# Performance work log

Measured on AMD Instinct MI355X. Metric: run time of the kernel, lower is better.

The kernel has to match this reference:

```python
import jax, jax.numpy as jnp
import numpy as np

K = 20        # kNN neighborhood size (args.k)
EPS = 1e-5    # BatchNorm eps
SLOPE = 0.2   # LeakyReLU negative slope
B, N = 8, 2048


def lrelu(x):
    return jnp.where(x >= 0, x, SLOPE * x)


def bn_cn(x):  # BatchNorm1d over [B, C, N] (training-mode batch stats, gamma=1, beta=0)
    m = jnp.mean(x, axis=(0, 2), keepdims=True)
    v = jnp.var(x, axis=(0, 2), keepdims=True)
    return (x - m) * jax.lax.rsqrt(v + EPS)


def bn_f(x):  # BatchNorm1d over [B, F]
    m = jnp.mean(x, axis=0, keepdims=True)
    v = jnp.var(x, axis=0, keepdims=True)
    return (x - m) * jax.lax.rsqrt(v + EPS)


def conv_bn(x, w):  # 1x1 Conv1d (no bias) + BN + LeakyReLU; x [B,C,N], w [O,C]
    return lrelu(bn_cn(jnp.einsum('oc,bcn->bon', w, x)))


def knn_idx(x, k):  # x [B,C,N] -> [B,N,k] nearest neighbors, self excluded
    sq = jnp.sum(x * x, axis=1)                                   # [B,N]
    pd = 2.0 * jnp.einsum('bcn,bcm->bnm', x, x) - sq[:, :, None] - sq[:, None, :]
    return jax.lax.top_k(pd, k + 1)[1][:, :, 1:]                  # drop self (max = 0)


def self_att(x, wq, wk, wv, wc):  # SelfAttention block (n_heads=1, scale_dot)
    idx = knn_idx(x, K)                                           # [B,N,K]
    feats = jnp.swapaxes(x, 1, 2)                                 # [B,N,C]
    nb = jax.vmap(lambda f, i: f[i])(feats, idx)                  # [B,N,K,C] gather
    E = wq.shape[0]
    q = feats @ wq.T                                              # [B,N,E]
    kk = nb @ wk.T                                                # [B,N,K,E]
    v = (nb - feats[:, :, None, :]) @ wv.T                        # [B,N,K,V]
    scores = jax.nn.softmax(jnp.einsum('bne,bnke->bnk', q, kk) / np.float32(np.sqrt(E)), axis=-1)
    out = jnp.einsum('bnk,bnkv->bnv', scores, v)                  # [B,N,V]
    res = conv_bn(jnp.swapaxes(out, 1, 2), wc)                    # [B,O,N]
    return jnp.concatenate([res, x], axis=1)


def setup_inputs() -> dict:
    key = jax.random.key(0)
    ks = jax.random.split(key, 32)
    w = lambda k, o, i: jax.random.normal(k, (o, i), jnp.float32) / np.float32(np.sqrt(i))
    d = {'x': jax.random.normal(ks[0], (B, 3, N), jnp.float32)}
    dims = {1: 3, 2: 64, 3: 64, 4: 128}
    j = 1
    for s, c in dims.items():
        for nm in ('wq', 'wk', 'wv', 'wc'):
            d[f'sa{s}_{nm}'] = w(ks[j], c, c); j += 1
    d['conv1_w'] = w(ks[17], 64, 6)
    d['conv2_w'] = w(ks[18], 64, 128)
    d['conv3_w'] = w(ks[19], 128, 128)
    d['conv4_w'] = w(ks[20], 256, 256)
    d['conv5_w'] = w(ks[21], 1024, 512)
    d['lin1_w'] = w(ks[22], 512, 2048); d['lin1_b'] = jnp.zeros((512,), jnp.float32)
    d['lin2_w'] = w(ks[23], 256, 512);  d['lin2_b'] = jnp.zeros((256,), jnp.float32)
    d['lin3_w'] = w(ks[24], 40, 256);   d['lin3_b'] = jnp.zeros((40,), jnp.float32)
    return d


def reference(x, sa1_wq, sa1_wk, sa1_wv, sa1_wc, sa2_wq, sa2_wk, sa2_wv, sa2_wc,
              sa3_wq, sa3_wk, sa3_wv, sa3_wc, sa4_wq, sa4_wk, sa4_wv, sa4_wc,
              conv1_w, conv2_w, conv3_w, conv4_w, conv5_w,
              lin1_w, lin1_b, lin2_w, lin2_b, lin3_w, lin3_b):
    h = self_att(x, sa1_wq, sa1_wk, sa1_wv, sa1_wc)        # [B,6,N]
    x1 = conv_bn(h, conv1_w)                               # [B,64,N]
    h = self_att(x1, sa2_wq, sa2_wk, sa2_wv, sa2_wc)       # [B,128,N]
    x2 = conv_bn(h, conv2_w)                               # [B,64,N]
    h = self_att(x2, sa3_wq, sa3_wk, sa3_wv, sa3_wc)       # [B,128,N]
    x3 = conv_bn(h, conv3_w)                               # [B,128,N]
    h = self_att(x3, sa4_wq, sa4_wk, sa4_wv, sa4_wc)       # [B,256,N]
    x4 = conv_bn(h, conv4_w)                               # [B,256,N]
    xc = jnp.concatenate([x1, x2, x3, x4], axis=1)         # [B,512,N]
    x5 = conv_bn(xc, conv5_w)                              # [B,1024,N]
    p = jnp.concatenate([jnp.max(x5, axis=2), jnp.mean(x5, axis=2)], axis=1)  # [B,2048]
    h = lrelu(bn_f(p @ lin1_w.T + lin1_b))                 # dropout = identity (eval)
    h = lrelu(bn_f(h @ lin2_w.T + lin2_b))
    return h @ lin3_w.T + lin3_b                           # [B,40]
```

## Files before the change

kernel.cpp:

```cpp
#include <hip/hip_runtime.h>
#include <math.h>

#define BB 8
#define NN 2048
#define KNB 20

typedef __attribute__((ext_vector_type(8))) short bf16x8;
typedef __attribute__((ext_vector_type(8))) _Float16 f16x8;
typedef __attribute__((ext_vector_type(4))) float f32x4;

__device__ inline unsigned short f2bf(float f) {
  union { float f; unsigned u; } v; v.f = f;
  unsigned r = v.u + 0x7FFF + ((v.u >> 16) & 1);
  return (unsigned short)(r >> 16);
}

__device__ inline float lrelu(float v) { return v >= 0.f ? v : 0.2f * v; }

template <bool F16SPLIT, bool BF16>
__global__ __launch_bounds__(256) void xprep_kernel(
    const float* __restrict__ in, int inBS, int C,
    float* __restrict__ xT, _Float16* __restrict__ hi, _Float16* __restrict__ lo,
    unsigned short* __restrict__ bf, float* __restrict__ sq) {
  __shared__ float tile[32][33];
// ... 358 lines not shown
    __syncthreads();
    atomicAdd(&gstats[o0 * 2 + tid], sb[tid]);
  }
}

__global__ __launch_bounds__(256, 2) void pd_mfma_sym_kernel(
    const _Float16* __restrict__ xhi, const _Float16* __restrict__ xlo, int C,
    const float* __restrict__ sq, float* __restrict__ P, int b_base) {
  const int bl = blockIdx.y;
  const int b = b_base + bl;
  int ti = 0, xx = blockIdx.x;
  while (xx >= 16 - ti) { xx -= 16 - ti; ++ti; }
  const int tj = ti + xx;
  const int n0 = ti * 128, m0 = tj * 128;
  const int tid = threadIdx.x;
  const int wave = tid >> 6, lane = tid & 63;
  const int wn_ = wave >> 1, wm_ = wave & 1;
  const int l16 = lane & 15, q = lane >> 4;
  __shared__ _Float16 Ah[4096], Al[4096], Bh[4096], Bl[4096];
  const _Float16* Ahg = xhi + ((size_t)b * NN + n0) * C;
  const _Float16* Alg = xlo + ((size_t)b * NN + n0) * C;
  const _Float16* Bhg = xhi + ((size_t)b * NN + m0) * C;
  const _Float16* Blg = xlo + ((size_t)b * NN + m0) * C;

  const int p0 = tid, p1 = tid + 256;
  const int r0 = ((p0 >> 6) << 4) | (p0 & 15), c0 = ((p0 >> 4) & 3) * 8;
  const int r1 = ((p1 >> 6) << 4) | (p1 & 15), c1 = ((p1 >> 4) & 3) * 8;

  f32x4 acc[4][4];
#pragma unroll
  for (int s = 0; s < 4; ++s)
#pragma unroll
    for (int t = 0; t < 4; ++t) acc[s][t] = (f32x4){0.f, 0.f, 0.f, 0.f};

  for (int k0 = 0; k0 < C; k0 += 32) {
    __syncthreads();
    *(f16x8*)&Ah[p0 * 8] = *(const f16x8*)(Ahg + (size_t)r0 * C + k0 + c0);
    *(f16x8*)&Ah[p1 * 8] = *(const f16x8*)(Ahg + (size_t)r1 * C + k0 + c1);
    *(f16x8*)&Al[p0 * 8] = *(const f16x8*)(Alg + (size_t)r0 * C + k0 + c0);
    *(f16x8*)&Al[p1 * 8] = *(const f16x8*)(Alg + (size_t)r1 * C + k0 + c1);
    *(f16x8*)&Bh[p0 * 8] = *(const f16x8*)(Bhg + (size_t)r0 * C + k0 + c0);
    *(f16x8*)&Bh[p1 * 8] = *(const f16x8*)(Bhg + (size_t)r1 * C + k0 + c1);
    *(f16x8*)&Bl[p0 * 8] = *(const f16x8*)(Blg + (size_t)r0 * C + k0 + c0);
    *(f16x8*)&Bl[p1 * 8] = *(const f16x8*)(Blg + (size_t)r1 * C + k0 + c1);
    __syncthreads();
    f16x8 ah[4], al[4], bh[4], blv[4];
#pragma unroll
    for (int s = 0; s < 4; ++s) {
      int pi = ((wn_ * 4 + s) * 64 + q * 16 + l16) * 8;
      ah[s] = *(const f16x8*)&Ah[pi];
      al[s] = *(const f16x8*)&Al[pi];
    }
#pragma unroll
    for (int t = 0; t < 4; ++t) {
      int pi = ((wm_ * 4 + t) * 64 + q * 16 + l16) * 8;
      bh[t] = *(const f16x8*)&Bh[pi];
      blv[t] = *(const f16x8*)&Bl[pi];
    }
#pragma unroll
    for (int s = 0; s < 4; ++s)
#pragma unroll
      for (int t = 0; t < 4; ++t) {
        acc[s][t] = __builtin_amdgcn_mfma_f32_16x16x32_f16(ah[s], bh[t], acc[s][t], 0, 0, 0);
        acc[s][t] = __builtin_amdgcn_mfma_f32_16x16x32_f16(ah[s], blv[t], acc[s][t], 0, 0, 0);
        acc[s][t] = __builtin_amdgcn_mfma_f32_16x16x32_f16(al[s], bh[t], acc[s][t], 0, 0, 0);
      }
  }
#pragma unroll
  for (int s = 0; s < 4; ++s)
#pragma unroll
    for (int t = 0; t < 4; ++t) {
      int col = m0 + wm_ * 64 + t * 16 + l16;
      float sqv = sq[b * NN + col];
      float* pp = P + ((size_t)bl * NN + n0 + wn_ * 64 + s * 16 + q * 4) * NN + col;
#pragma unroll
      for (int r = 0; r < 4; ++r) pp[(size_t)r * NN] = 2.f * acc[s][t][r] - sqv;
    }
  if (ti != tj) {
#pragma unroll
    for (int s = 0; s < 4; ++s) {
      int nb = n0 + wn_ * 64 + s * 16 + q * 4;
      float4 sqn = *(const float4*)&sq[b * NN + nb];
#pragma unroll
      for (int t = 0; t < 4; ++t) {
        int m = m0 + wm_ * 64 + t * 16 + l16;
        f32x4 ov;
        ov[0] = 2.f * acc[s][t][0] - sqn.x;
        ov[1] = 2.f * acc[s][t][1] - sqn.y;
        ov[2] = 2.f * acc[s][t][2] - sqn.z;
        ov[3] = 2.f * acc[s][t][3] - sqn.w;
        *(f32x4*)&P[((size_t)bl * NN + m) * NN + nb] = ov;
      }
    }
  }
}

__global__ __launch_bounds__(256) void topk_bsort_kernel(const float* __restrict__ P,
                                                         int* __restrict__ idx_out, int b_base) {
  const int wave = threadIdx.x >> 6;
  const int lane = threadIdx.x & 63;
  const int n = blockIdx.x * 4 + wave;
  const int bl = blockIdx.y;
  const int b = b_base + bl;
  const float4* rp = (const float4*)(P + ((size_t)bl * NN + n) * NN);
  unsigned key[32];
#pragma unroll
  for (int q = 0; q < 8; ++q) {
    float4 vv = rp[q * 64 + lane];
    int mb = q * 256 + lane * 4;
    float fv[4] = {vv.x, vv.y, vv.z, vv.w};
#pragma unroll
    for (int j = 0; j < 4; ++j) {
      unsigned u = __float_as_uint(fv[j]);
      unsigned mask = (unsigned)(((int)u) >> 31) | 0x80000000u;
      unsigned sl = (unsigned)(q * 4 + j);
      key[q * 4 + j] = (mb + j == n) ? sl : (((u ^ mask) & 0xFFFFFFE0u) | sl);
    }
  }
#pragma unroll
  for (int k = 2; k <= 32; k <<= 1) {
#pragma unroll
    for (int j = k >> 1; j > 0; j >>= 1) {
#pragma unroll
      for (int i = 0; i < 32; ++i) {
        int l = i ^ j;
        if (l > i) {
          unsigned ka = key[i], kb = key[l];
          unsigned mx = ka > kb ? ka : kb;
          unsigned mn = ka > kb ? kb : ka;
          if ((i & k) == 0) { key[i] = mx; key[l] = mn; }
          else              { key[i] = mn; key[l] = mx; }
        }
      }
    }
  }
  int* op = idx_out + (size_t)(b * NN + n) * KNB;
  for (int k = 0; k < KNB; ++k) {
    unsigned best = key[0];
#pragma unroll
    for (int s = 32; s > 0; s >>= 1) {
      unsigned o = (unsigned)__shfl_xor((int)best, s);
      best = best > o ? best : o;
    }
    unsigned long long bal = __ballot(key[0] == best);
    if (lane == (int)__ffsll(bal) - 1) {
      unsigned sl = key[0] & 31u;
      op[k] = (int)((sl >> 2) * 256u + (unsigned)lane * 4u + (sl & 3u));
#pragma unroll
      for (int j = 0; j < 20; ++j) key[j] = key[j + 1];
    }
  }
}

__global__ __launch_bounds__(256) void topk_c3_kernel(const float* __restrict__ xs4,
                                                      int* __restrict__ idx_out) {
  const int wave = threadIdx.x >> 6;
  const int lane = threadIdx.x & 63;
  const int n = blockIdx.x * 4 + wave;
  const int b = blockIdx.y;
  const float4* xp = (const float4*)(xs4 + (size_t)b * NN * 4);
  float4 me = xp[n];
  float tx = 2.f * me.x, ty = 2.f * me.y, tz = 2.f * me.z;
  unsigned key[32];
#pragma unroll
  for (int s = 0; s < 32; ++s) {
    int m = s * 64 + lane;
    float4 c = xp[m];
    float pd = tx * c.x + ty * c.y + tz * c.z - c.w;
    unsigned u = __float_as_uint(pd);
    unsigned mask = (unsigned)(((int)u) >> 31) | 0x80000000u;
    key[s] = (m == n) ? (unsigned)s : ((((u ^ mask) & 0xFFFFFFE0u)) | (unsigned)s);
  }
#pragma unroll
  for (int k = 2; k <= 32; k <<= 1) {
#pragma unroll
    for (int j = k >> 1; j > 0; j >>= 1) {
#pragma unroll
      for (int i = 0; i < 32; ++i) {
        int l = i ^ j;
        if (l > i) {
          unsigned ka = key[i], kb = key[l];
          unsigned mx = ka > kb ? ka : kb;
          unsigned mn = ka > kb ? kb : ka;
          if ((i & k) == 0) { key[i] = mx; key[l] = mn; }
          else              { key[i] = mn; key[l] = mx; }
        }
      }
    }
  }
  int* op = idx_out + (size_t)(b * NN + n) * KNB;
  for (int k = 0; k < KNB; ++k) {
    unsigned best = key[0];
#pragma unroll
    for (int s = 32; s > 0; s >>= 1) {
      unsigned o = (unsigned)__shfl_xor((int)best, s);
      best = best > o ? best : o;
    }
    unsigned long long bal = __ballot(key[0] == best);
    if (lane == (int)__ffsll(bal) - 1) {
      unsigned sl = key[0] & 31u;
      op[k] = (int)(sl * 64u + (unsigned)lane);
#pragma unroll
      for (int j = 0; j < 20; ++j) key[j] = key[j + 1];
    }
  }
}

__global__ __launch_bounds__(256) void sa1_fused_kernel(
    const float* __restrict__ xs4, const int* __restrict__ idx,
    const float* __restrict__ M, const float* __restrict__ W,
    float* __restrict__ z) {
  __shared__ float Ms[9], Ws9[9];
  int t = threadIdx.x;
  if (t < 9) Ms[t] = M[t];
  else if (t < 18) Ws9[t - 9] = W[t - 9];
  __syncthreads();
  int gid = blockIdx.x * 256 + t;
  int b = gid >> 11, n = gid & (NN - 1);
  const float4* xp = (const float4*)(xs4 + (size_t)b * NN * 4);
  float4 me = xp[n];
  float u0 = Ms[0] * me.x + Ms[1] * me.y + Ms[2] * me.z;
  float u1 = Ms[3] * me.x + Ms[4] * me.y + Ms[5] * me.z;
  float u2 = Ms[6] * me.x + Ms[7] * me.y + Ms[8] * me.z;
  const float scale = 0.57735026919f;
  const int* ip = idx + (size_t)gid * KNB;
  float nbx[KNB], nby[KNB], nbz[KNB], sc[KNB];
#pragma unroll
  for (int k = 0; k < KNB; ++k) {
    int m = ip[k] & (NN - 1);
    float4 c = xp[m];
    nbx[k] = c.x; nby[k] = c.y; nbz[k] = c.z;
    sc[k] = (c.x * u0 + c.y * u1 + c.z * u2) * scale;
  }
  float mx = sc[0];
#pragma unroll
  for (int k = 1; k < KNB; ++k) mx = fmaxf(mx, sc[k]);
  float sum = 0.f;
#pragma unroll
  for (int k = 0; k < KNB; ++k) { sc[k] = expf(sc[k] - mx); sum += sc[k]; }
  float inv = 1.f / sum;
  float a0 = 0.f, a1 = 0.f, a2 = 0.f;
#pragma unroll
  for (int k = 0; k < KNB; ++k) { a0 += sc[k] * nbx[k]; a1 += sc[k] * nby[k]; a2 += sc[k] * nbz[k]; }
  a0 = a0 * inv - me.x; a1 = a1 * inv - me.y; a2 = a2 * inv - me.z;
  float* zb = z + (size_t)b * 3 * NN;
  zb[n]          = Ws9[0] * a0 + Ws9[1] * a1 + Ws9[2] * a2;
  zb[NN + n]     = Ws9[3] * a0 + Ws9[4] * a1 + Ws9[5] * a2;
  zb[2 * NN + n] = Ws9[6] * a0 + Ws9[7] * a1 + Ws9[8] * a2;
}

template <bool BT, bool TOUT>
__global__ __launch_bounds__(256, 2) void conv_gemm_kernel(
    const float* __restrict__ in, int inBS, int C, int O,
    const float* __restrict__ w, float* __restrict__ z) {
  const int b = blockIdx.z;
  const int n0 = blockIdx.x * 64, o0 = blockIdx.y * 64;
  const int tid = threadIdx.x;
  const int tm = tid & 15, tn = tid >> 4;
  __shared__ float Ws[16][68];
  __shared__ float Xs[16][64];
  const float* ib = in + (size_t)b * inBS;
  float acc[4][4];
#pragma unroll
  for (int i = 0; i < 4; ++i)
#pragma unroll
    for (int j = 0; j < 4; ++j) acc[i][j] = 0.f;

  for (int k0 = 0; k0 < C; k0 += 16) {
    __syncthreads();
#pragma unroll
    for (int it = 0; it < 4; ++it) {
      int i = it * 256 + tid;
      if (BT) {
        int kc = i & 15, nl = i >> 4;
        Xs[kc][nl] = ((k0 + kc) < C) ? ib[(size_t)(n0 + nl) * C + k0 + kc] : 0.f;
      } else {
        int kc = i >> 6, nl = i & 63;
        Xs[kc][nl] = ((k0 + kc) < C) ? ib[(size_t)(k0 + kc) * NN + n0 + nl] : 0.f;
      }
      int ol = i >> 4, kc2 = i & 15;
      Ws[kc2][ol] = ((o0 + ol) < O && (k0 + kc2) < C) ? w[(size_t)(o0 + ol) * C + k0 + kc2] : 0.f;
    }
    __syncthreads();
#pragma unroll
    for (int kc = 0; kc < 16; ++kc) {
      float4 a = *(const float4*)&Ws[kc][tn * 4];
      float4 bv = *(const float4*)&Xs[kc][tm * 4];
      acc[0][0] += a.x * bv.x; acc[0][1] += a.x * bv.y; acc[0][2] += a.x * bv.z; acc[0][3] += a.x * bv.w;
      acc[1][0] += a.y * bv.x; acc[1][1] += a.y * bv.y; acc[1][2] += a.y * bv.z; acc[1][3] += a.y * bv.w;
      acc[2][0] += a.z * bv.x; acc[2][1] += a.z * bv.y; acc[2][2] += a.z * bv.z; acc[2][3] += a.z * bv.w;
      acc[3][0] += a.w * bv.x; acc[3][1] += a.w * bv.y; acc[3][2] += a.w * bv.z; acc[3][3] += a.w * bv.w;
    }
  }
  if (TOUT) {
#pragma unroll
    for (int j = 0; j < 4; ++j) {
      int n = n0 + tm * 4 + j;
      int ob = o0 + tn * 4;
      if (ob < O) {
        float4 ov;
        ov.x = acc[0][j]; ov.y = acc[1][j]; ov.z = acc[2][j]; ov.w = acc[3][j];
        *(float4*)&z[((size_t)b * NN + n) * O + ob] = ov;
      }
    }
  } else {
#pragma unroll
    for (int i = 0; i < 4; ++i) {
      int o = o0 + tn * 4 + i;
      if (o < O) {
        float4 ov;
        ov.x = acc[i][0]; ov.y = acc[i][1]; ov.z = acc[i][2]; ov.w = acc[i][3];
        *(float4*)&z[((size_t)b * O + o) * NN + n0 + tm * 4] = ov;
      }
    }
  }
}

__global__ __launch_bounds__(256, 2) void conv_gemm128_db_kernel(
    const float* __restrict__ in, int inBS, int C, int O,
    const float* __restrict__ w, float* __restrict__ z) {
  const int b = blockIdx.z;
  const int n0 = blockIdx.x * 128, o0 = blockIdx.y * 128;
  const int tid = threadIdx.x;
  const int tm = tid & 15, tn = tid >> 4;
  __shared__ float Xs[2][16][128];
  __shared__ float Ws[2][16][132];
  const float* ib = in + (size_t)b * inBS;
  float acc[8][8];
#pragma unroll
  for (int i = 0; i < 8; ++i)
#pragma unroll
    for (int j = 0; j < 8; ++j) acc[i][j] = 0.f;

  float4 xr[2], wr[2];
  auto load_tile = [&](int k0) {
#pragma unroll
    for (int it = 0; it < 2; ++it) {
      int i = it * 256 + tid;
      int kc = i >> 5, c4 = i & 31;
      xr[it] = ((k0 + kc) < C) ? *(const float4*)&ib[(size_t)(k0 + kc) * NN + n0 + c4 * 4]
                               : make_float4(0.f, 0.f, 0.f, 0.f);
      int ol = i >> 2, kq = i & 3;
      wr[it] = ((k0 + kq * 4) < C) ? *(const float4*)&w[(size_t)(o0 + ol) * C + k0 + kq * 4]
                                   : make_float4(0.f, 0.f, 0.f, 0.f);
    }
  };
  auto store_tile = [&](int buf) {
#pragma unroll
    for (int it = 0; it < 2; ++it) {
      int i = it * 256 + tid;
      int kc = i >> 5, c4 = i & 31;
      *(float4*)&Xs[buf][kc][c4 * 4] = xr[it];
      int ol = i >> 2, kq = i & 3;
      Ws[buf][kq * 4 + 0][ol] = wr[it].x;
      Ws[buf][kq * 4 + 1][ol] = wr[it].y;
      Ws[buf][kq * 4 + 2][ol] = wr[it].z;
      Ws[buf][kq * 4 + 3][ol] = wr[it].w;
    }
  };

  load_tile(0);
  store_tile(0);
  int cur = 0;
  for (int k0 = 0; k0 < C; k0 += 16) {
    bool more = (k0 + 16) < C;
    if (more) load_tile(k0 + 16);
    __syncthreads();
#pragma unroll
    for (int kc = 0; kc < 16; ++kc) {
      float4 a0 = *(const float4*)&Ws[cur][kc][tn * 4];
      float4 a1 = *(const float4*)&Ws[cur][kc][64 + tn * 4];
      float4 b0 = *(const float4*)&Xs[cur][kc][tm * 4];
      float4 b1 = *(const float4*)&Xs[cur][kc][64 + tm * 4];
      float ar[8] = {a0.x, a0.y, a0.z, a0.w, a1.x, a1.y, a1.z, a1.w};
      float br[8] = {b0.x, b0.y, b0.z, b0.w, b1.x, b1.y, b1.z, b1.w};
#pragma unroll
      for (int i = 0; i < 8; ++i)
#pragma unroll
        for (int j = 0; j < 8; ++j) acc[i][j] += ar[i] * br[j];
    }
    if (more) store_tile(cur ^ 1);
    cur ^= 1;
  }
#pragma unroll
  for (int h = 0; h < 2; ++h)
#pragma unroll
    for (int i = 0; i < 4; ++i) {
      int r = h * 4 + i;
      int o = o0 + h * 64 + tn * 4 + i;
      float* zrow = &z[((size_t)b * O + o) * NN + n0];
      float4 o0v, o1v;
      o0v.x = acc[r][0]; o0v.y = acc[r][1]; o0v.z = acc[r][2]; o0v.w = acc[r][3];
      o1v.x = acc[r][4]; o1v.y = acc[r][5]; o1v.z = acc[r][6]; o1v.w = acc[r][7];
      *(float4*)&zrow[tm * 4] = o0v;
      *(float4*)&zrow[64 + tm * 4] = o1v;
    }
}

template <int C, bool BF16OUT>
__global__ __launch_bounds__(256) void att_wave_reg_kernel(
    const float* __restrict__ xT, const float* __restrict__ UT,
    const int* __restrict__ idx, float* __restrict__ AGGt,
    unsigned short* __restrict__ AGGtb) {
  const int lane = threadIdx.x & 63;
  const int gid = blockIdx.x * 4 + (threadIdx.x >> 6);
  const int n = gid & (NN - 1);
  const int b = gid >> 11;
  const float* xTb = xT + (size_t)b * NN * C;
  int nv = idx[(size_t)gid * KNB + (lane < KNB ? lane : 0)];
  float u0 = UT[(size_t)gid * C + lane];
  float u1;
  if (C == 128) u1 = UT[(size_t)gid * C + 64 + lane];
  float v0[KNB], v1[KNB], p[KNB];
#pragma unroll
  for (int k = 0; k < KNB; ++k) {
    int m = __shfl(nv, k) & (NN - 1);
    v0[k] = xTb[(size_t)m * C + lane];
    if (C == 128) v1[k] = xTb[(size_t)m * C + 64 + lane];
  }
#pragma unroll
  for (int k = 0; k < KNB; ++k) {
    float a = v0[k] * u0;
    if (C == 128) a += v1[k] * u1;
    p[k] = a;
  }
#pragma unroll
  for (int k = 0; k < KNB; ++k) {
#pragma unroll
    for (int s = 32; s > 0; s >>= 1) p[k] += __shfl_xor(p[k], s);
  }
  const float scale = (C == 128) ? 0.088388347648318447f : 0.125f;
  float mx = p[0];
#pragma unroll
  for (int k = 1; k < KNB; ++k) mx = fmaxf(mx, p[k]);
  float sum = 0.f;
#pragma unroll
  for (int k = 0; k < KNB; ++k) {
    p[k] = expf((p[k] - mx) * scale);
    sum += p[k];
  }
  float inv = 1.f / sum;
  float a0 = 0.f, a1 = 0.f;
#pragma unroll
  for (int k = 0; k < KNB; ++k) {
    a0 += p[k] * v0[k];
    if (C == 128) a1 += p[k] * v1[k];
  }
  float r0 = a0 * inv - xTb[(size_t)n * C + lane];
  float r1;
  if (C == 128) r1 = a1 * inv - xTb[(size_t)n * C + 64 + lane];
  if (BF16OUT) {
    AGGtb[(size_t)gid * C + lane] = f2bf(r0);
    if (C == 128) AGGtb[(size_t)gid * C + 64 + lane] = f2bf(r1);
  } else {
    AGGt[(size_t)gid * C + lane] = r0;
    if (C == 128) AGGt[(size_t)gid * C + 64 + lane] = r1;
  }
}

template <bool PRE>
__global__ __launch_bounds__(256) void bn_fused_kernel(const float* __restrict__ z, int O,
                                                       float* __restrict__ out, int outBS, int c0,
                                                       const float* __restrict__ gs) {
  int o = blockIdx.x;
  int tid = threadIdx.x;
  float m, r;
  if (PRE) {
    float s = gs[o * 2], s2 = gs[o * 2 + 1];
    m = s / (BB * NN);
    float var = s2 / (BB * NN) - m * m;
    r = rsqrtf(var + 1e-5f);
  } else {
    __shared__ float s1[256], s2[256];
    __shared__ float smv, srv;
    float a1 = 0.f, a2 = 0.f;
    for (int i = tid; i < BB * 512; i += 256) {
      int b = i >> 9, n4 = i & 511;
      float4 v = *(const float4*)&z[((size_t)b * O + o) * NN + n4 * 4];
      a1 += v.x + v.y + v.z + v.w;
      a2 += v.x * v.x + v.y * v.y + v.z * v.z + v.w * v.w;
    }
    s1[tid] = a1; s2[tid] = a2;
    __syncthreads();
    for (int st = 128; st > 0; st >>= 1) {
      if (tid < st) { s1[tid] += s1[tid + st]; s2[tid] += s2[tid + st]; }
      __syncthreads();
    }
    if (tid == 0) {
      float mm = s1[0] / (BB * NN);
      float var = s2[0] / (BB * NN) - mm * mm;
      smv = mm; srv = rsqrtf(var + 1e-5f);
    }
    __syncthreads();
    m = smv; r = srv;
  }
  for (int i = tid; i < BB * 512; i += 256) {
    int b = i >> 9, n4 = i & 511;
    float4 v = *(const float4*)&z[((size_t)b * O + o) * NN + n4 * 4];
    float4 ov;
    ov.x = lrelu((v.x - m) * r); ov.y = lrelu((v.y - m) * r);
    ov.z = lrelu((v.z - m) * r); ov.w = lrelu((v.w - m) * r);
    *(float4*)&out[(size_t)b * outBS + (size_t)(c0 + o) * NN + n4 * 4] = ov;
  }
}

__global__ __launch_bounds__(256) void bn_copy_kernel(const float* __restrict__ z, int O,
                                                      const float* __restrict__ xin, int xbs,
                                                      float* __restrict__ out) {
  int o = blockIdx.x;
  int tid = threadIdx.x;
  int outBS = 2 * O * NN;
  if (o >= O) {
    int c = o - O;
    for (int i = tid; i < BB * 512; i += 256) {
      int b = i >> 9, n4 = i & 511;
      *(float4*)&out[(size_t)b * outBS + (size_t)o * NN + n4 * 4] =
          *(const float4*)&xin[(size_t)b * xbs + (size_t)c * NN + n4 * 4];
    }
    return;
  }
  __shared__ float s1[256], s2[256];
  __shared__ float smv, srv;
  float a1 = 0.f, a2 = 0.f;
  for (int i = tid; i < BB * 512; i += 256) {
    int b = i >> 9, n4 = i & 511;
    float4 v = *(const float4*)&z[((size_t)b * O + o) * NN + n4 * 4];
    a1 += v.x + v.y + v.z + v.w;
    a2 += v.x * v.x + v.y * v.y + v.z * v.z + v.w * v.w;
  }
  s1[tid] = a1; s2[tid] = a2;
  __syncthreads();
  for (int st = 128; st > 0; st >>= 1) {
    if (tid < st) { s1[tid] += s1[tid + st]; s2[tid] += s2[tid + st]; }
    __syncthreads();
  }
  if (tid == 0) {
    float m = s1[0] / (BB * NN);
    float var = s2[0] / (BB * NN) - m * m;
    smv = m; srv = rsqrtf(var + 1e-5f);
  }
  __syncthreads();
  float m = smv, r = srv;
  for (int i = tid; i < BB * 512; i += 256) {
    int b = i >> 9, n4 = i & 511;
    float4 v = *(const float4*)&z[((size_t)b * O + o) * NN + n4 * 4];
    float4 ov;
    ov.x = lrelu((v.x - m) * r); ov.y = lrelu((v.y - m) * r);
    ov.z = lrelu((v.z - m) * r); ov.w = lrelu((v.w - m) * r);
    *(float4*)&out[(size_t)b * outBS + (size_t)o * NN + n4 * 4] = ov;
  }
}

template <bool PRE>
__global__ __launch_bounds__(256) void bn_pool_kernel(const float* __restrict__ z,
                                                      float* __restrict__ p,
                                                      const float* __restrict__ gs) {
  int o = blockIdx.x;
  int tid = threadIdx.x;
  float m, r;
  if (PRE) {
    float s = gs[o * 2], s2 = gs[o * 2 + 1];
    m = s / (BB * NN);
    float var = s2 / (BB * NN) - m * m;
    r = rsqrtf(var + 1e-5f);
  } else {
    __shared__ float s1[256], s2[256];
    __shared__ float smv, srv;
    float a1 = 0.f, a2 = 0.f;
    for (int i = tid; i < BB * 512; i += 256) {
      int b = i >> 9, n4 = i & 511;
      float4 v = *(const float4*)&z[((size_t)b * 1024 + o) * NN + n4 * 4];
      a1 += v.x + v.y + v.z + v.w;
      a2 += v.x * v.x + v.y * v.y + v.z * v.z + v.w * v.w;
    }
    s1[tid] = a1; s2[tid] = a2;
    __syncthreads();
    for (int st = 128; st > 0; st >>= 1) {
      if (tid < st) { s1[tid] += s1[tid + st]; s2[tid] += s2[tid + st]; }
      __syncthreads();
    }
    if (tid == 0) {
      float mm = s1[0] / (BB * NN);
      float var = s2[0] / (BB * NN) - mm * mm;
      smv = mm; srv = rsqrtf(var + 1e-5f);
    }
    __syncthreads();
    m = smv; r = srv;
  }
  int b = tid >> 5, l = tid & 31;
  const float* zp = z + ((size_t)b * 1024 + o) * NN;
  float mx = -INFINITY, sm = 0.f;
  for (int j = l; j < 512; j += 32) {
    float4 v = *(const float4*)&zp[j * 4];
    float vx = lrelu((v.x - m) * r), vy = lrelu((v.y - m) * r);
    float vz = lrelu((v.z - m) * r), vw = lrelu((v.w - m) * r);
    mx = fmaxf(mx, fmaxf(fmaxf(vx, vy), fmaxf(vz, vw)));
    sm += vx + vy + vz + vw;
  }
#pragma unroll
  for (int s = 16; s > 0; s >>= 1) {
    mx = fmaxf(mx, __shfl_xor(mx, s));
    sm += __shfl_xor(sm, s);
  }
  if (l == 0) {
    p[b * 2048 + o] = mx;
    p[b * 2048 + 1024 + o] = sm * (1.f / NN);
  }
}

__global__ __launch_bounds__(64) void linear_kernel(const float* __restrict__ in, int IN, int OUT,
                                                    const float* __restrict__ w,
                                                    const float* __restrict__ bias,
                                                    float* __restrict__ out) {
  int o = blockIdx.x;
  int b = o / OUT, f = o % OUT;
  const float* ip = in + (size_t)b * IN;
  const float* wp = w + (size_t)f * IN;
  float a = 0.f;
  for (int i = threadIdx.x; i < IN; i += 64) a += ip[i] * wp[i];
#pragma unroll
  for (int s = 32; s > 0; s >>= 1) a += __shfl_down(a, s);
  if (threadIdx.x == 0) out[o] = a + bias[f];
}

__global__ __launch_bounds__(256) void bnf_kernel(float* __restrict__ t, int F) {
  int f = blockIdx.x * blockDim.x + threadIdx.x;
  if (f >= F) return;
  float s = 0.f, s2 = 0.f;
  for (int b = 0; b < BB; ++b) { float v = t[b * F + f]; s += v; s2 += v * v; }
  float m = s * (1.f / BB);
  float var = s2 * (1.f / BB) - m * m;
  float r = rsqrtf(var + 1e-5f);
  for (int b = 0; b < BB; ++b) {
    float v = (t[b * F + f] - m) * r;
    t[b * F + f] = v >= 0.f ? v : 0.2f * v;
  }
}


struct SAW { const float *wq, *wk, *wv, *wc; };

static inline void run_conv(const float* in, int inBS, int C, int O, const float* w,
                            float* z, hipStream_t st) {
  if (O % 128 == 0)
    conv_gemm128_db_kernel<<<dim3(NN / 128, O / 128, BB), 256, 0, st>>>(in, inBS, C, O, w, z);
  else
    conv_gemm_kernel<false, false><<<dim3(NN / 64, (O + 63) / 64, BB), 256, 0, st>>>(in, inBS, C, O, w, z);
}

template <int C, bool MFMA>
static inline void run_sa(const float* xin, int xbs,
                          float* xT, float* UT, float* AGGt, float* z, float* h,
                          float* sq, int* idx,
                          const float* M, const float* WCV,
                          const unsigned short* Mb, const unsigned short* wcvb,
                          unsigned short* xTb, unsigned short* AGGtb,
                          _Float16* xhi, _Float16* xlo,
                          float* D, int nbatch, hipStream_t st) {
  static_assert(C % 32 == 0, "run_sa requires C % 32 == 0");
  xprep_kernel<true, MFMA><<<dim3(NN / 32, C / 32, BB), 256, 0, st>>>(
      xin, xbs, C, xT, xhi, xlo, xTb, sq);
  for (int bb = 0; bb < BB; bb += nbatch) {
    int nbc = (BB - bb) < nbatch ? (BB - bb) : nbatch;
    pd_mfma_sym_kernel<<<dim3(136, nbc), 256, 0, st>>>(xhi, xlo, C, sq, D, bb);
    topk_bsort_kernel<<<dim3(NN / 4, nbc), 256, 0, st>>>(D, idx, bb);
  }
  if (MFMA) {
    mfma_gemm_lds_kernel<true, false><<<dim3(NN / 128, C / 128, BB), 256, 0, st>>>(
        (const unsigned short*)Mb, xTb, UT, C, C, nullptr);
    att_wave_reg_kernel<C, true><<<BB * NN / 4, 256, 0, st>>>(xT, UT, idx, nullptr, AGGtb);
    mfma_gemm_lds_kernel<false, false><<<dim3(NN / 128, C / 128, BB), 256, 0, st>>>(
        (const unsigned short*)wcvb, AGGtb, z, C, C, nullptr);
  } else {
    conv_gemm_kernel<false, true><<<dim3(NN / 64, C / 64, BB), 256, 0, st>>>(xin, xbs, C, C, M, UT);
    att_wave_reg_kernel<C, false><<<BB * NN / 4, 256, 0, st>>>(xT, UT, idx, AGGt, nullptr);
    conv_gemm_kernel<true, false><<<dim3(NN / 64, C / 64, BB), 256, 0, st>>>(AGGt, NN * C, C, C, WCV, z);
  }
  bn_copy_kernel<<<2 * C, 256, 0, st>>>(z, C, xin, xbs, h);
}

static inline void run_sa3(const float* xin, float* z, float* h, float* xs4, int* idx,
                           const float* M, const float* WCV, hipStream_t st) {
  xprep3_kernel<<<dim3(NN / 256, 1, BB), 256, 0, st>>>(xin, xs4);
  topk_c3_kernel<<<dim3(NN / 4, BB), 256, 0, st>>>(xs4, idx);
  sa1_fused_kernel<<<BB * NN / 256, 256, 0, st>>>(xs4, idx, M, WCV, z);
  bn_copy_kernel<<<6, 256, 0, st>>>(z, 3, xin, 3 * NN, h);
}

static inline void run_conv_bn(const float* in, int inBS, int Cin, int O, const float* w,
                               float* z, float* out, int outBS, int c0, hipStream_t st) {
  run_conv(in, inBS, Cin, O, w, z, st);
  bn_fused_kernel<false><<<O, 256, 0, st>>>(z, O, out, outBS, c0, nullptr);
}

extern "C" void kernel_launch(void* const* d_in, const int* in_sizes, int n_in,
                              void* d_out, int out_size, void* d_ws, size_t ws_size,
                              hipStream_t stream) {
  const float* x = (const float*)d_in[0];
  SAW sa1{(const float*)d_in[1], (const float*)d_in[2], (const float*)d_in[3], (const float*)d_in[4]};
  SAW sa2{(const float*)d_in[5], (const float*)d_in[6], (const float*)d_in[7], (const float*)d_in[8]};
  SAW sa3{(const float*)d_in[9], (const float*)d_in[10], (const float*)d_in[11], (const float*)d_in[12]};
  SAW sa4{(const float*)d_in[13], (const float*)d_in[14], (const float*)d_in[15], (const float*)d_in[16]};
  const float* conv1_w = (const float*)d_in[17];
  const float* conv2_w = (const float*)d_in[18];
  const float* conv3_w = (const float*)d_in[19];
  const float* conv4_w = (const float*)d_in[20];
  const float* conv5_w = (const float*)d_in[21];
  const float* lin1_w = (const float*)d_in[22];
  const float* lin1_b = (const float*)d_in[23];
  const float* lin2_w = (const float*)d_in[24];
  const float* lin2_b = (const float*)d_in[25];
  const float* lin3_w = (const float*)d_in[26];
  const float* lin3_b = (const float*)d_in[27];

  char* ws = (char*)d_ws;
  size_t off = 0;
  auto take = [&](size_t bytes) -> void* {
    void* p = ws + off;
    off += (bytes + 255) & ~(size_t)255;
    return p;
  };
  float* sqR  = (float*)take((size_t)3 * BB * NN * 4);
  float* statsR = (float*)take((size_t)(256 + 1024) * 2 * 4);
  float* xs4  = (float*)take((size_t)BB * NN * 4 * 4);
  int*   idx  = (int*)take((size_t)BB * NN * KNB * 4);
  float* Mall = (float*)take((size_t)4 * 128 * 128 * 4);
  float* Wall = (float*)take((size_t)4 * 128 * 128 * 4);
  unsigned short* Mb4   = (unsigned short*)take((size_t)128 * 128 * 2);
  unsigned short* wcvb4 = (unsigned short*)take((size_t)128 * 128 * 2);
  unsigned short* w4b  = (unsigned short*)take((size_t)256 * 256 * 2);
  unsigned short* w5b  = (unsigned short*)take((size_t)1024 * 512 * 2);
  float* U    = (float*)take((size_t)BB * 128 * NN * 4);
  float* AGG  = (float*)take((size_t)BB * 128 * NN * 4);
  float* h    = (float*)take((size_t)BB * 256 * NN * 4);
  float* z    = (float*)take((size_t)BB * 1024 * NN * 4);
  float* xc   = (float*)take((size_t)BB * 512 * NN * 4);
  float* p    = (float*)take((size_t)BB * 2048 * 4);
  float* t1   = (float*)take((size_t)BB * 512 * 4);
  float* t2   = (float*)take((size_t)BB * 256 * 4);
  (void)n_in; (void)in_sizes; (void)out_size;

  float* M1 = Mall + 0 * 16384; float* W1 = Wall + 0 * 16384;
  float* M2 = Mall + 1 * 16384; float* W2 = Wall + 1 * 16384;
  float* M3 = Mall + 2 * 16384; float* W3 = Wall + 2 * 16384;
  float* M4 = Mall + 3 * 16384; float* W4 = Wall + 3 * 16384;
  float* stats4 = statsR;
  float* stats5 = statsR + 256 * 2;

  float* xT = AGG;
  float* AGGt64 = AGG + (size_t)BB * NN * 64;
  float* UT = h;
  unsigned short* xTb   = (unsigned short*)((char*)h + (size_t)BB * 128 * NN * 4);
  unsigned short* AGGtb = (unsigned short*)((char*)z + (size_t)16 * 1024 * 1024);
  unsigned short* hTb   = (unsigned short*)U;
  unsigned short* xcTb  = (unsigned short*)U;
  _Float16* xhi = (_Float16*)h;
  _Float16* xlo = (_Float16*)((char*)h + (size_t)BB * NN * 128 * 2);

  size_t dfull = (size_t)BB * NN * NN * 4;
  bool fullD = (ws_size > off + dfull + 4096);
  float* D = fullD ? (float*)take(dfull) : z;
  int nbatch = fullD ? BB : 4;

  hipMemsetAsync(sqR, 0, (size_t)3 * BB * NN * 4 + (size_t)(256 + 1024) * 2 * 4, stream);
  weight_prep_kernel<<<5 + 2048 + 2048 + 8192 + 256 + 2048, 256, 0, stream>>>(
      sa1.wq, sa1.wk, sa1.wv, sa1.wc, sa2.wq, sa2.wk, sa2.wv, sa2.wc,
      sa3.wq, sa3.wk, sa3.wv, sa3.wc, sa4.wq, sa4.wk, sa4.wv, sa4.wc,
      conv4_w, conv5_w, M1, W1, M2, W2, M3, W3, M4, W4, Mb4, wcvb4, w4b, w5b);

  run_sa3(x, z, h, xs4, idx, M1, W1, stream);
  run_conv_bn(h, 6 * NN, 6, 64, conv1_w, z, xc, 512 * NN, 0, stream);
  run_sa<64, false>(xc + 0 * NN, 512 * NN, xT, UT, AGGt64, z, h,
                    sqR + 0 * BB * NN, idx, M2, W2, nullptr, nullptr, xTb, AGGtb, xhi, xlo,
                    D, nbatch, stream);
  run_conv_bn(h, 128 * NN, 128, 64, conv2_w, z, xc, 512 * NN, 64, stream);
  run_sa<64, false>(xc + 64 * NN, 512 * NN, xT, UT, AGGt64, z, h,
                    sqR + 1 * BB * NN, idx, M3, W3, nullptr, nullptr, xTb, AGGtb, xhi, xlo,
                    D, nbatch, stream);
  run_conv_bn(h, 128 * NN, 128, 128, conv3_w, z, xc, 512 * NN, 128, stream);
  run_sa<128, true>(xc + 128 * NN, 512 * NN, xT, UT, nullptr, z, h,
                    sqR + 2 * BB * NN, idx, M4, W4, Mb4, wcvb4, xTb, AGGtb, xhi, xlo,
                    D, nbatch, stream);
  transpose_bf16_kernel<<<dim3(NN / 32, 8, BB), 256, 0, stream>>>(h, 256 * NN, 256, NN, hTb);
  mfma_gemm_lds_kernel<false, true><<<dim3(NN / 128, 2, BB), 256, 0, stream>>>(
      w4b, hTb, z, 256, 256, stats4);
  bn_fused_kernel<true><<<256, 256, 0, stream>>>(z, 256, xc, 512 * NN, 256, stats4);
  transpose_bf16_kernel<<<dim3(NN / 32, 16, BB), 256, 0, stream>>>(xc, 512 * NN, 512, NN, xcTb);
  mfma_gemm_n256_kernel<<<dim3(NN / 256, 8, BB), 256, 0, stream>>>(
      w5b, xcTb, z, 1024, 512, stats5);
  bn_pool_kernel<true><<<1024, 256, 0, stream>>>(z, p, stats5);
  linear_kernel<<<BB * 512, 64, 0, stream>>>(p, 2048, 512, lin1_w, lin1_b, t1);
  bnf_kernel<<<2, 256, 0, stream>>>(t1, 512);
  linear_kernel<<<BB * 256, 64, 0, stream>>>(t1, 512, 256, lin2_w, lin2_b, t2);
  bnf_kernel<<<1, 256, 0, stream>>>(t2, 256);
  linear_kernel<<<BB * 40, 64, 0, stream>>>(t2, 256, 40, lin3_w, lin3_b, (float*)d_out);
}
```

Measured before the change: 828.6 us.

## Fuse BN statistics into conv epilogues, merge sa1 topk+attention, fuse linear+BN

Conv GEMM kernels now accumulate per-channel sum and sum-of-squares in their epilogue, using shared then global atomics. This lets the BN kernels skip a separate full reduction pass over z. The stage-1 top-k and attention kernels are merged so each wave computes softmax aggregation from its own neighbor lanes, removing the idx round-trip. The linear and batch-norm-over-features kernels are fused into one kernel per layer, cutting launches. Atomic float accumulation introduces nondeterministic ordering, and the E[x^2]-m^2 variance form may lose precision.

Result: slower. 866.5 us (+4.6%).

```diff
diff --git a/kernel.cpp b/kernel.cpp
--- a/kernel.cpp
+++ b/kernel.cpp
@@ -534,12 +534,17 @@
   }
 }
 
-__global__ __launch_bounds__(256) void topk_c3_kernel(const float* __restrict__ xs4,
-                                                      int* __restrict__ idx_out) {
+__global__ __launch_bounds__(256) void sa1_topk_att_kernel(
+    const float* __restrict__ xs4, const float* __restrict__ M,
+    const float* __restrict__ W, float* __restrict__ z) {
+  __shared__ float Ms[9], Ws9[9];
+  if (threadIdx.x < 9) Ms[threadIdx.x] = M[threadIdx.x];
+  else if (threadIdx.x < 18) Ws9[threadIdx.x - 9] = W[threadIdx.x - 9];
+  __syncthreads();
   const int wave = threadIdx.x >> 6;
   const int lane = threadIdx.x & 63;
-  const int n = blockIdx.x * 4 + wave;
-  const int b = blockIdx.y;
+  const int gid = blockIdx.x * 4 + wave;
+  const int b = gid >> 11, n = gid & (NN - 1);
   const float4* xp = (const float4*)(xs4 + (size_t)b * NN * 4);
   float4 me = xp[n];
   float tx = 2.f * me.x, ty = 2.f * me.y, tz = 2.f * me.z;
@@ -570,7 +575,7 @@
       }
     }
   }
-  int* op = idx_out + (size_t)(b * NN + n) * KNB;
+  int mymk = 0;
   for (int k = 0; k < KNB; ++k) {
     unsigned best = key[0];
 #pragma unroll
@@ -579,62 +584,50 @@
       best = best > o ? best : o;
     }
     unsigned long long bal = __ballot(key[0] == best);
-    if (lane == (int)__ffsll(bal) - 1) {
-      unsigned sl = key[0] & 31u;
-      op[k] = (int)(sl * 64u + (unsigned)lane);
+    int owner = (int)__ffsll(bal) - 1;
+    int mk = (int)((best & 31u) * 64u + (unsigned)owner);
+    if (lane == k) mymk = mk;
+    if (lane == owner) {
 #pragma unroll
       for (int j = 0; j < 20; ++j) key[j] = key[j + 1];
     }
   }
-}
-
-__global__ __launch_bounds__(256) void sa1_fused_kernel(
-    const float* __restrict__ xs4, const int* __restrict__ idx,
-    const float* __restrict__ M, const float* __restrict__ W,
-    float* __restrict__ z) {
-  __shared__ float Ms[9], Ws9[9];
-  int t = threadIdx.x;
-  if (t < 9) Ms[t] = M[t];
-  else if (t < 18) Ws9[t - 9] = W[t - 9];
-  __syncthreads();
-  int gid = blockIdx.x * 256 + t;
-  int b = gid >> 11, n = gid & (NN - 1);
-  const float4* xp = (const float4*)(xs4 + (size_t)b * NN * 4);
-  float4 me = xp[n];
   float u0 = Ms[0] * me.x + Ms[1] * me.y + Ms[2] * me.z;
   float u1 = Ms[3] * me.x + Ms[4] * me.y + Ms[5] * me.z;
   float u2 = Ms[6] * me.x + Ms[7] * me.y + Ms[8] * me.z;
   const float scale = 0.57735026919f;
-  const int* ip = idx + (size_t)gid * KNB;
-  float nbx[KNB], nby[KNB], nbz[KNB], sc[KNB];
-#pragma unroll
-  for (int k = 0; k < KNB; ++k) {
-    int m = ip[k] & (NN - 1);
-    float4 c = xp[m];
-    nbx[k] = c.x; nby[k] = c.y; nbz[k] = c.z;
-    sc[k] = (c.x * u0 + c.y * u1 + c.z * u2) * scale;
-  }
-  float mx = sc[0];
-#pragma unroll
-  for (int k = 1; k < KNB; ++k) mx = fmaxf(mx, sc[k]);
-  float sum = 0.f;
-#pragma unroll
-  for (int k = 0; k < KNB; ++k) { sc[k] = expf(sc[k] - mx); sum += sc[k]; }
-  float inv = 1.f / sum;
-  float a0 = 0.f, a1 = 0.f, a2 = 0.f;
-#pragma unroll
-  for (int k = 0; k < KNB; ++k) { a0 += sc[k] * nbx[k]; a1 += sc[k] * nby[k]; a2 += sc[k] * nbz[k]; }
-  a0 = a0 * inv - me.x; a1 = a1 * inv - me.y; a2 = a2 * inv - me.z;
-  float* zb = z + (size_t)b * 3 * NN;
-  zb[n]          = Ws9[0] * a0 + Ws9[1] * a1 + Ws9[2] * a2;
-  zb[NN + n]     = Ws9[3] * a0 + Ws9[4] * a1 + Ws9[5] * a2;
-  zb[2 * NN + n] = Ws9[6] * a0 + Ws9[7] * a1 + Ws9[8] * a2;
-}
-
-template <bool BT, bool TOUT>
+  float4 c = xp[mymk & (NN - 1)];
+  float sv = (lane < KNB) ? (c.x * u0 + c.y * u1 + c.z * u2) * scale : -INFINITY;
+  float mx = sv;
+#pragma unroll
+  for (int s = 32; s > 0; s >>= 1) mx = fmaxf(mx, __shfl_xor(mx, s));
+  float e = (lane < KNB) ? expf(sv - mx) : 0.f;
+  float sum = e;
+#pragma unroll
+  for (int s = 32; s > 0; s >>= 1) sum += __shfl_xor(sum, s);
+  float p = e / sum;
+  float a0 = (lane < KNB) ? p * c.x : 0.f;
+  float a1 = (lane < KNB) ? p * c.y : 0.f;
+  float a2 = (lane < KNB) ? p * c.z : 0.f;
+#pragma unroll
+  for (int s = 32; s > 0; s >>= 1) {
+    a0 += __shfl_xor(a0, s);
+    a1 += __shfl_xor(a1, s);
+    a2 += __shfl_xor(a2, s);
+  }
+  if (lane == 0) {
+    a0 -= me.x; a1 -= me.y; a2 -= me.z;
+    float* zb = z + (size_t)b * 3 * NN;
+    zb[n]          = Ws9[0] * a0 + Ws9[1] * a1 + Ws9[2] * a2;
+    zb[NN + n]     = Ws9[3] * a0 + Ws9[4] * a1 + Ws9[5] * a2;
+    zb[2 * NN + n] = Ws9[6] * a0 + Ws9[7] * a1 + Ws9[8] * a2;
+  }
+}
+
+template <bool BT, bool TOUT, bool STATS>
 __global__ __launch_bounds__(256, 2) void conv_gemm_kernel(
     const float* __restrict__ in, int inBS, int C, int O,
-    const float* __restrict__ w, float* __restrict__ z) {
+    const float* __restrict__ w, float* __restrict__ z, float* __restrict__ gstats) {
   const int b = blockIdx.z;
   const int n0 = blockIdx.x * 64, o0 = blockIdx.y * 64;
   const int tid = threadIdx.x;
@@ -696,11 +689,31 @@
       }
     }
   }
-}
-
+  if (STATS) {
+    __shared__ float sb[128];
+    if (tid < 128) sb[tid] = 0.f;
+    __syncthreads();
+#pragma unroll
+    for (int i = 0; i < 4; ++i) {
+      int o = o0 + tn * 4 + i;
+      if (o < O) {
+        float s = acc[i][0] + acc[i][1] + acc[i][2] + acc[i][3];
+        float q2 = acc[i][0] * acc[i][0] + acc[i][1] * acc[i][1]
+                 + acc[i][2] * acc[i][2] + acc[i][3] * acc[i][3];
+        atomicAdd(&sb[(tn * 4 + i) * 2], s);
+        atomicAdd(&sb[(tn * 4 + i) * 2 + 1], q2);
+      }
+    }
+    __syncthreads();
+    if (tid < 128 && (o0 + (tid >> 1)) < O)
+      atomicAdd(&gstats[(size_t)(o0 + (tid >> 1)) * 2 + (tid & 1)], sb[tid]);
+  }
+}
+
+template <bool STATS>
 __global__ __launch_bounds__(256, 2) void conv_gemm128_db_kernel(
     const float* __restrict__ in, int inBS, int C, int O,
-    const float* __restrict__ w, float* __restrict__ z) {
+    const float* __restrict__ w, float* __restrict__ z, float* __restrict__ gstats) {
   const int b = blockIdx.z;
   const int n0 = blockIdx.x * 128, o0 = blockIdx.y * 128;
   const int tid = threadIdx.x;
@@ -777,6 +790,25 @@
       *(float4*)&zrow[tm * 4] = o0v;
       *(float4*)&zrow[64 + tm * 4] = o1v;
     }
+  if (STATS) {
+    __shared__ float sb[256];
+    sb[tid] = 0.f;
+    __syncthreads();
+#pragma unroll
+    for (int h = 0; h < 2; ++h)
+#pragma unroll
+      for (int i = 0; i < 4; ++i) {
+        int r = h * 4 + i;
+        int lch = h * 64 + tn * 4 + i;
+        float s = 0.f, q2 = 0.f;
+#pragma unroll
+        for (int j = 0; j < 8; ++j) { float v = acc[r][j]; s += v; q2 += v * v; }
+        atomicAdd(&sb[lch * 2], s);
+        atomicAdd(&sb[lch * 2 + 1], q2);
+      }
+    __syncthreads();
+    atomicAdd(&gstats[(size_t)o0 * 2 + tid], sb[tid]);
+  }
 }
 
 template <int C, bool BF16OUT>
@@ -886,9 +918,11 @@
   }
 }
 
+template <bool PRE>
 __global__ __launch_bounds__(256) void bn_copy_kernel(const float* __restrict__ z, int O,
                                                       const float* __restrict__ xin, int xbs,
-                                                      float* __restrict__ out) {
+                                                      float* __restrict__ out,
+                                                      const float* __restrict__ gs) {
   int o = blockIdx.x;
   int tid = threadIdx.x;
   int outBS = 2 * O * NN;
@@ -901,28 +935,36 @@
     }
     return;
   }
-  __shared__ float s1[256], s2[256];
-  __shared__ float smv, srv;
-  float a1 = 0.f, a2 = 0.f;
-  for (int i = tid; i < BB * 512; i += 256) {
-    int b = i >> 9, n4 = i & 511;
-    float4 v = *(const float4*)&z[((size_t)b * O + o) * NN + n4 * 4];
-    a1 += v.x + v.y + v.z + v.w;
-    a2 += v.x * v.x + v.y * v.y + v.z * v.z + v.w * v.w;
-  }
-  s1[tid] = a1; s2[tid] = a2;
-  __syncthreads();
-  for (int st = 128; st > 0; st >>= 1) {
-    if (tid < st) { s1[tid] += s1[tid + st]; s2[tid] += s2[tid + st]; }
-    __syncthreads();
-  }
-  if (tid == 0) {
-    float m = s1[0] / (BB * NN);
-    float var = s2[0] / (BB * NN) - m * m;
-    smv = m; srv = rsqrtf(var + 1e-5f);
-  }
-  __syncthreads();
-  float m = smv, r = srv;
+  float m, r;
+  if (PRE) {
+    float s = gs[o * 2], s2 = gs[o * 2 + 1];
+    m = s / (BB * NN);
+    float var = s2 / (BB * NN) - m * m;
+    r = rsqrtf(var + 1e-5f);
+  } else {
+    __shared__ float s1[256], s2[256];
+    __shared__ float smv, srv;
+    float a1 = 0.f, a2 = 0.f;
+    for (int i = tid; i < BB * 512; i += 256) {
+      int b = i >> 9, n4 = i & 511;
+      float4 v = *(const float4*)&z[((size_t)b * O + o) * NN + n4 * 4];
+      a1 += v.x + v.y + v.z + v.w;
+      a2 += v.x * v.x + v.y * v.y + v.z * v.z + v.w * v.w;
+    }
+    s1[tid] = a1; s2[tid] = a2;
+    __syncthreads();
+    for (int st = 128; st > 0; st >>= 1) {
+      if (tid < st) { s1[tid] += s1[tid + st]; s2[tid] += s2[tid + st]; }
+      __syncthreads();
+    }
+    if (tid == 0) {
+      float mm = s1[0] / (BB * NN);
+      float var = s2[0] / (BB * NN) - mm * mm;
+      smv = mm; srv = rsqrtf(var + 1e-5f);
+    }
+    __syncthreads();
+    m = smv; r = srv;
+  }
   for (int i = tid; i < BB * 512; i += 256) {
     int b = i >> 9, n4 = i & 511;
     float4 v = *(const float4*)&z[((size_t)b * O + o) * NN + n4 * 4];
@@ -990,32 +1032,37 @@
   }
 }
 
-__global__ __launch_bounds__(64) void linear_kernel(const float* __restrict__ in, int IN, int OUT,
-                                                    const float* __restrict__ w,
-                                                    const float* __restrict__ bias,
-                                                    float* __restrict__ out) {
-  int o = blockIdx.x;
-  int b = o / OUT, f = o % OUT;
-  const float* ip = in + (size_t)b * IN;
+template <bool BN>
+__global__ __launch_bounds__(256) void linear_bnf_kernel(
+    const float* __restrict__ in, int IN, int OUT,
+    const float* __restrict__ w, const float* __restrict__ bias,
+    float* __restrict__ out) {
+  int f = blockIdx.x;
+  int g = threadIdx.x >> 5, l = threadIdx.x & 31;
   const float* wp = w + (size_t)f * IN;
+  const float* ip = in + (size_t)g * IN;
   float a = 0.f;
-  for (int i = threadIdx.x; i < IN; i += 64) a += ip[i] * wp[i];
-#pragma unroll
-  for (int s = 32; s > 0; s >>= 1) a += __shfl_down(a, s);
-  if (threadIdx.x == 0) out[o] = a + bias[f];
-}
-
-__global__ __launch_bounds__(256) void bnf_kernel(float* __restrict__ t, int F) {
-  int f = blockIdx.x * blockDim.x + threadIdx.x;
-  if (f >= F) return;
-  float s = 0.f, s2 = 0.f;
-  for (int b = 0; b < BB; ++b) { float v = t[b * F + f]; s += v; s2 += v * v; }
-  float m = s * (1.f / BB);
-  float var = s2 * (1.f / BB) - m * m;
-  float r = rsqrtf(var + 1e-5f);
-  for (int b = 0; b < BB; ++b) {
-    float v = (t[b * F + f] - m) * r;
-    t[b * F + f] = v >= 0.f ? v : 0.2f * v;
+  for (int i = l; i < IN; i += 32) a += ip[i] * wp[i];
+#pragma unroll
+  for (int s = 16; s > 0; s >>= 1) a += __shfl_xor(a, s);
+  __shared__ float sv[8];
+  if (l == 0) sv[g] = a + bias[f];
+  __syncthreads();
+  if (threadIdx.x < 8) {
+    float v;
+    if (BN) {
+      float m = 0.f, s2 = 0.f;
+#pragma unroll
+      for (int bb = 0; bb < 8; ++bb) { float x = sv[bb]; m += x; s2 += x * x; }
+      m *= 0.125f;
+      float var = s2 * 0.125f - m * m;
+      float r = rsqrtf(var + 1e-5f);
+      v = (sv[threadIdx.x] - m) * r;
+      v = v >= 0.f ? v : 0.2f * v;
+    } else {
+      v = sv[threadIdx.x];
+    }
+    out[(size_t)threadIdx.x * OUT + f] = v;
   }
 }
 
@@ -1023,17 +1070,17 @@
 struct SAW { const float *wq, *wk, *wv, *wc; };
 
 static inline void run_conv(const float* in, int inBS, int C, int O, const float* w,
-                            float* z, hipStream_t st) {
+                            float* z, float* gstats, hipStream_t st) {
   if (O % 128 == 0)
-    conv_gemm128_db_kernel<<<dim3(NN / 128, O / 128, BB), 256, 0, st>>>(in, inBS, C, O, w, z);
+    conv_gemm128_db_kernel<true><<<dim3(NN / 128, O / 128, BB), 256, 0, st>>>(in, inBS, C, O, w, z, gstats);
   else
-    conv_gemm_kernel<false, false><<<dim3(NN / 64, (O + 63) / 64, BB), 256, 0, st>>>(in, inBS, C, O, w, z);
+    conv_gemm_kernel<false, false, true><<<dim3(NN / 64, (O + 63) / 64, BB), 256, 0, st>>>(in, inBS, C, O, w, z, gstats);
 }
 
 template <int C, bool MFMA>
 static inline void run_sa(const float* xin, int xbs,
                           float* xT, float* UT, float* AGGt, float* z, float* h,
-                          float* sq, int* idx,
+                          float* sq, int* idx, float* stz,
                           const float* M, const float* WCV,
                           const unsigned short* Mb, const unsigned short* wcvb,
                           unsigned short* xTb, unsigned short* AGGtb,
@@ -1051,28 +1098,28 @@
     mfma_gemm_lds_kernel<true, false><<<dim3(NN / 128, C / 128, BB), 256, 0, st>>>(
         (const unsigned short*)Mb, xTb, UT, C, C, nullptr);
     att_wave_reg_kernel<C, true><<<BB * NN / 4, 256, 0, st>>>(xT, UT, idx, nullptr, AGGtb);
-    mfma_gemm_lds_kernel<false, false><<<dim3(NN / 128, C / 128, BB), 256, 0, st>>>(
-        (const unsigned short*)wcvb, AGGtb, z, C, C, nullptr);
+    mfma_gemm_lds_kernel<false, true><<<dim3(NN / 128, C / 128, BB), 256, 0, st>>>(
+        (const unsigned short*)wcvb, AGGtb, z, C, C, stz);
   } else {
-    conv_gemm_kernel<false, true><<<dim3(NN / 64, C / 64, BB), 256, 0, st>>>(xin, xbs, C, C, M, UT);
+    conv_gemm_kernel<false, true, false><<<dim3(NN / 64, C / 64, BB), 256, 0, st>>>(xin, xbs, C, C, M, UT, nullptr);
     att_wave_reg_kernel<C, false><<<BB * NN / 4, 256, 0, st>>>(xT, UT, idx, AGGt, nullptr);
-    conv_gemm_kernel<true, false><<<dim3(NN / 64, C / 64, BB), 256, 0, st>>>(AGGt, NN * C, C, C, WCV, z);
-  }
-  bn_copy_kernel<<<2 * C, 256, 0, st>>>(z, C, xin, xbs, h);
-}
-
-static inline void run_sa3(const float* xin, float* z, float* h, float* xs4, int* idx,
+    conv_gemm_kernel<true, false, true><<<dim3(NN / 64, C / 64, BB), 256, 0, st>>>(AGGt, NN * C, C, C, WCV, z, stz);
+  }
+  bn_copy_kernel<true><<<2 * C, 256, 0, st>>>(z, C, xin, xbs, h, stz);
+}
+
+static inline void run_sa3(const float* xin, float* z, float* h, float* xs4,
                            const float* M, const float* WCV, hipStream_t st) {
   xprep3_kernel<<<dim3(NN / 256, 1, BB), 256, 0, st>>>(xin, xs4);
-  topk_c3_kernel<<<dim3(NN / 4, BB), 256, 0, st>>>(xs4, idx);
-  sa1_fused_kernel<<<BB * NN / 256, 256, 0, st>>>(xs4, idx, M, WCV, z);
-  bn_copy_kernel<<<6, 256, 0, st>>>(z, 3, xin, 3 * NN, h);
+  sa1_topk_att_kernel<<<BB * NN / 4, 256, 0, st>>>(xs4, M, WCV, z);
+  bn_copy_kernel<false><<<6, 256, 0, st>>>(z, 3, xin, 3 * NN, h, nullptr);
 }
 
 static inline void run_conv_bn(const float* in, int inBS, int Cin, int O, const float* w,
-                               float* z, float* out, int outBS, int c0, hipStream_t st) {
-  run_conv(in, inBS, Cin, O, w, z, st);
-  bn_fused_kernel<false><<<O, 256, 0, st>>>(z, O, out, outBS, c0, nullptr);
+                               float* z, float* out, int outBS, int c0, float* gstats,
+                               hipStream_t st) {
+  run_conv(in, inBS, Cin, O, w, z, gstats, st);
+  bn_fused_kernel<true><<<O, 256, 0, st>>>(z, O, out, outBS, c0, gstats);
 }
 
 extern "C" void kernel_launch(void* const* d_in, const int* in_sizes, int n_in,
@@ -1103,7 +1150,7 @@
     return p;
   };
   float* sqR  = (float*)take((size_t)3 * BB * NN * 4);
-  float* statsR = (float*)take((size_t)(256 + 1024) * 2 * 4);
+  float* statsR = (float*)take((size_t)1792 * 2 * 4);
   float* xs4  = (float*)take((size_t)BB * NN * 4 * 4);
   int*   idx  = (int*)take((size_t)BB * NN * KNB * 4);
   float* Mall = (float*)take((size_t)4 * 128 * 128 * 4);
@@ -1126,8 +1173,14 @@
   float* M2 = Mall + 1 * 16384; float* W2 = Wall + 1 * 16384;
   float* M3 = Mall + 2 * 16384; float* W3 = Wall + 2 * 16384;
   float* M4 = Mall + 3 * 16384; float* W4 = Wall + 3 * 16384;
-  float* stats4 = statsR;
-  float* stats5 = statsR + 256 * 2;
+  float* stc1 = statsR;
+  float* stc2 = stc1 + 64 * 2;
+  float* stc3 = stc2 + 64 * 2;
+  float* st4  = stc3 + 128 * 2;
+  float* st5  = st4 + 256 * 2;
+  float* stz2 = st5 + 1024 * 2;
+  float* stz3 = stz2 + 64 * 2;
+  float* stz4 = stz3 + 64 * 2;
 
   float* xT = AGG;
   float* AGGt64 = AGG + (size_t)BB * NN * 64;
@@ -1144,36 +1197,34 @@
   float* D = fullD ? (float*)take(dfull) : z;
   int nbatch = fullD ? BB : 4;
 
-  hipMemsetAsync(sqR, 0, (size_t)3 * BB * NN * 4 + (size_t)(256 + 1024) * 2 * 4, stream);
+  hipMemsetAsync(sqR, 0, (size_t)((char*)(statsR + 1792 * 2) - (char*)sqR), stream);
   weight_prep_kernel<<<5 + 2048 + 2048 + 8192 + 256 + 2048, 256, 0, stream>>>(
       sa1.wq, sa1.wk, sa1.wv, sa1.wc, sa2.wq, sa2.wk, sa2.wv, sa2.wc,
       sa3.wq, sa3.wk, sa3.wv, sa3.wc, sa4.wq, sa4.wk, sa4.wv, sa4.wc,
       conv4_w, conv5_w, M1, W1, M2, W2, M3, W3, M4, W4, Mb4, wcvb4, w4b, w5b);
 
-  run_sa3(x, z, h, xs4, idx, M1, W1, stream);
-  run_conv_bn(h, 6 * NN, 6, 64, conv1_w, z, xc, 512 * NN, 0, stream);
+  run_sa3(x, z, h, xs4, M1, W1, stream);
+  run_conv_bn(h, 6 * NN, 6, 64, conv1_w, z, xc, 512 * NN, 0, stc1, stream);
   run_sa<64, false>(xc + 0 * NN, 512 * NN, xT, UT, AGGt64, z, h,
-                    sqR + 0 * BB * NN, idx, M2, W2, nullptr, nullptr, xTb, AGGtb, xhi, xlo,
-                    D, nbatch, stream);
-  run_conv_bn(h, 128 * NN, 128, 64, conv2_w, z, xc, 512 * NN, 64, stream);
+                    sqR + 0 * BB * NN, idx, stz2, M2, W2, nullptr, nullptr, xTb, AGGtb,
+                    xhi, xlo, D, nbatch, stream);
+  run_conv_bn(h, 128 * NN, 128, 64, conv2_w, z, xc, 512 * NN, 64, stc2, stream);
   run_sa<64, false>(xc + 64 * NN, 512 * NN, xT, UT, AGGt64, z, h,
-                    sqR + 1 * BB * NN, idx, M3, W3, nullptr, nullptr, xTb, AGGtb, xhi, xlo,
-                    D, nbatch, stream);
-  run_conv_bn(h, 128 * NN, 128, 128, conv3_w, z, xc, 512 * NN, 128, stream);
+                    sqR + 1 * BB * NN, idx, stz3, M3, W3, nullptr, nullptr, xTb, AGGtb,
+                    xhi, xlo, D, nbatch, stream);
+  run_conv_bn(h, 128 * NN, 128, 128, conv3_w, z, xc, 512 * NN, 128, stc3, stream);
   run_sa<128, true>(xc + 128 * NN, 512 * NN, xT, UT, nullptr, z, h,
-                    sqR + 2 * BB * NN, idx, M4, W4, Mb4, wcvb4, xTb, AGGtb, xhi, xlo,
-                    D, nbatch, stream);
+                    sqR + 2 * BB * NN, idx, stz4, M4, W4, Mb4, wcvb4, xTb, AGGtb,
+                    xhi, xlo, D, nbatch, stream);
   transpose_bf16_kernel<<<dim3(NN / 32, 8, BB), 256, 0, stream>>>(h, 256 * NN, 256, NN, hTb);
   mfma_gemm_lds_kernel<false, true><<<dim3(NN / 128, 2, BB), 256, 0, stream>>>(
-      w4b, hTb, z, 256, 256, stats4);
-  bn_fused_kernel<true><<<256, 256, 0, stream>>>(z, 256, xc, 512 * NN, 256, stats4);
+      w4b, hTb, z, 256, 256, st4);
+  bn_fused_kernel<true><<<256, 256, 0, stream>>>(z, 256, xc, 512 * NN, 256, st4);
   transpose_bf16_kernel<<<dim3(NN / 32, 16, BB), 256, 0, stream>>>(xc, 512 * NN, 512, NN, xcTb);
   mfma_gemm_n256_kernel<<<dim3(NN / 256, 8, BB), 256, 0, stream>>>(
-      w5b, xcTb, z, 1024, 512, stats5);
-  bn_pool_kernel<true><<<1024, 256, 0, stream>>>(z, p, stats5);
-  linear_kernel<<<BB * 512, 64, 0, stream>>>(p, 2048, 512, lin1_w, lin1_b, t1);
-  bnf_kernel<<<2, 256, 0, stream>>>(t1, 512);
-  linear_kernel<<<BB * 256, 64, 0, stream>>>(t1, 512, 256, lin2_w, lin2_b, t2);
-  bnf_kernel<<<1, 256, 0, stream>>>(t2, 256);
-  linear_kernel<<<BB * 40, 64, 0, stream>>>(t2, 256, 40, lin3_w, lin3_b, (float*)d_out);
-}
+      w5b, xcTb, z, 1024, 512, st5);
+  bn_pool_kernel<true><<<1024, 256, 0, stream>>>(z, p, st5);
+  linear_bnf_kernel<true><<<512, 256, 0, stream>>>(p, 2048, 512, lin1_w, lin1_b, t1);
+  linear_bnf_kernel<true><<<256, 256, 0, stream>>>(t1, 512, 256, lin2_w, lin2_b, t2);
+  linear_bnf_kernel<false><<<40, 256, 0, stream>>>(t2, 256, 40, lin3_w, lin3_b, (float*)d_out);
+}
```
